# Optimization experiments

Measured on AMD Instinct MI355X. Metric: run time of the kernel, lower is better.

Reference implementation:

```python
import jax, jax.numpy as jnp
import numpy as np


def _gcn_smooth(X, src, dst, d_inv_sqrt, n):
    """Symmetric-normalized GCN smoothing: D^-1/2 (A + I) D^-1/2 X,
    with undirected edges given as (src, dst) pairs (applied both ways)."""
    norm = d_inv_sqrt[src] * d_inv_sqrt[dst]            # [E]
    out = jax.ops.segment_sum(X[src] * norm[:, None], dst, num_segments=n)
    out = out + jax.ops.segment_sum(X[dst] * norm[:, None], src, num_segments=n)
    out = out + X * (d_inv_sqrt * d_inv_sqrt)[:, None]  # self loops
    return out


def setup_inputs() -> dict:
    key = jax.random.key(0)
    k1, k2, k3, k4, k5 = jax.random.split(key, 5)
    N, E, C_in, C_hid, C_out = 50000, 800000, 128, 64, 40
    X = jax.random.normal(k1, (N, C_in), dtype=jnp.float32)
    edge_index = jax.random.randint(k2, (2, E), 0, N, dtype=jnp.int32)
    s1 = 1.0 / np.sqrt(C_in)
    s2 = 1.0 / np.sqrt(C_hid)
    W1 = jax.random.uniform(k3, (C_in, C_hid), jnp.float32, -s1, s1)
    b1 = jax.random.uniform(k4, (C_hid,), jnp.float32, -s1, s1)
    W2 = jax.random.uniform(k5, (C_hid, C_out), jnp.float32, -s2, s2)
    b2 = jax.random.uniform(jax.random.fold_in(key, 7), (C_out,), jnp.float32, -s2, s2)
    return {"X": X, "W1": W1, "b1": b1, "W2": W2, "b2": b2, "edge_index": edge_index}


def reference(X, W1, b1, W2, b2, edge_index):
    n = X.shape[0]
    src, dst = edge_index[0], edge_index[1]
    ones = jnp.ones(src.shape[0], dtype=X.dtype)
    deg = (1.0
           + jax.ops.segment_sum(ones, dst, num_segments=n)
           + jax.ops.segment_sum(ones, src, num_segments=n))  # deg of A + I
    d_inv_sqrt = jax.lax.rsqrt(deg)

    # Layer 1: theta -> smoothing -> relu (dropout is identity in eval)
    h = X @ W1 + b1
    h = _gcn_smooth(h, src, dst, d_inv_sqrt, n)
    out1 = jax.nn.relu(h)

    # Layer 2 (is_last): theta -> smoothing
    h2 = out1 @ W2 + b2
    out2 = _gcn_smooth(h2, src, dst, d_inv_sqrt, n)
    return (out1, out2)
```

## Files before the change

kernel.cpp:

```cpp
#include <hip/hip_runtime.h>


#define B1 256
#define BT 1024
#define GROWS 512
#define BUCK_SHIFT 6
#define CAP 4096
#define STAGE 8192
#define WK 136
#define WK2 72

typedef float f32x4 __attribute__((ext_vector_type(4)));
typedef short bf16x8 __attribute__((ext_vector_type(8)));

union Frag { unsigned int u[4]; bf16x8 v; };

__device__ __forceinline__ unsigned int cvt_pk_bf16(float a, float b) {
    unsigned int r;
    asm("v_cvt_pk_bf16_f32 %0, %1, %2" : "=v"(r) : "v"(a), "v"(b));
    return r;
}

__device__ __forceinline__ float bf_lo(unsigned int u) {
    return __uint_as_float(u << 16);
}
__device__ __forceinline__ float bf_hi(unsigned int u) {
    return __uint_as_float(u & 0xffff0000u);
}

__device__ __forceinline__ bf16x8 ld_frag(const unsigned short* p) {
    uint4 t = *reinterpret_cast<const uint4*>(p);
    Frag f; f.u[0] = t.x; f.u[1] = t.y; f.u[2] = t.z; f.u[3] = t.w;
    return f.v;
}

__device__ __forceinline__ void make_frags(const float4 a, const float4 b,
                                           bf16x8& hi8, bf16x8& lo8) {
    Frag hi, lo;
    hi.u[0] = cvt_pk_bf16(a.x, a.y);
    hi.u[1] = cvt_pk_bf16(a.z, a.w);
    hi.u[2] = cvt_pk_bf16(b.x, b.y);
    hi.u[3] = cvt_pk_bf16(b.z, b.w);
    lo.u[0] = cvt_pk_bf16(a.x - __uint_as_float(hi.u[0] << 16),
                          a.y - __uint_as_float(hi.u[0] & 0xffff0000u));
    lo.u[1] = cvt_pk_bf16(a.z - __uint_as_float(hi.u[1] << 16),
                          a.w - __uint_as_float(hi.u[1] & 0xffff0000u));
    lo.u[2] = cvt_pk_bf16(b.x - __uint_as_float(hi.u[2] << 16),
                          b.y - __uint_as_float(hi.u[2] & 0xffff0000u));
    lo.u[3] = cvt_pk_bf16(b.z - __uint_as_float(hi.u[3] << 16),
                          b.w - __uint_as_float(hi.u[3] & 0xffff0000u));
    hi8 = hi.v; lo8 = lo.v;
}

__global__ __launch_bounds__(BT) void k_build_gemm1(
        const int* __restrict__ src, const int* __restrict__ dst,
        int* __restrict__ cursors, unsigned int* __restrict__ binned,
        const float* __restrict__ X, const float* __restrict__ W1,
        const float* __restrict__ b1, unsigned short* __restrict__ hub,
        int E, int nbuck, int chunk, int N) {
    __shared__ __align__(16) char smem[49152];

    if (blockIdx.x < B1) {
        int* lh    = (int*)smem;
        int* lscan = lh + 1024;
        int* sbuf  = lscan + 1024;
        int* lbase = sbuf + 1024;
        unsigned int* stage = (unsigned int*)(lbase + 1024);

        const int t = threadIdx.x;
        lh[t] = 0;
        __syncthreads();

        int e0 = blockIdx.x * chunk;
        int e1 = min(e0 + chunk, E);
        int es[4], eds[4];
        #pragma unroll
        for (int i = 0; i < 4; ++i) {
            int e = e0 + t + i * BT;
            if (e < e1) {
                int s = src[e], d = dst[e];
                es[i] = s; eds[i] = d;
                atomicAdd(&lh[s >> BUCK_SHIFT], 1);
                atomicAdd(&lh[d >> BUCK_SHIFT], 1);
            }
        }
        __syncthreads();

        int cntv = lh[t];
        int* bufA = sbuf; int* bufB = lscan;
        bufA[t] = cntv;
        __syncthreads();
        #pragma unroll
        for (int w = 1; w < 1024; w <<= 1) {
            int x = bufA[t];
            if (t >= w) x += bufA[t - w];
            bufB[t] = x;
            __syncthreads();
            int* tmp = bufA; bufA = bufB; bufB = tmp;
        }
        int excl = bufA[t] - cntv;
        lscan[t] = excl;
        int rel = (t < nbuck && cntv > 0) ? atomicAdd(&cursors[t], cntv) : 0;
        lbase[t] = t * CAP + rel;
        lh[t] = excl;
        __syncthreads();

        #pragma unroll
        for (int i = 0; i < 4; ++i) {
            int e = e0 + t + i * BT;
            if (e < e1) {
                unsigned int s = (unsigned int)es[i];
                unsigned int d = (unsigned int)eds[i];
                int ps = atomicAdd(&lh[s >> BUCK_SHIFT], 1);
                stage[ps] = (s << 16) | d;
                int pd = atomicAdd(&lh[d >> BUCK_SHIFT], 1);
                stage[pd] = (d << 16) | s;
            }
        }
        __syncthreads();

        int total = 2 * (e1 - e0);
        for (int i = t; i < total; i += BT) {
            unsigned int v = stage[i];
            int b = (v >> 16) >> BUCK_SHIFT;
            int gpos = lbase[b] + (i - lscan[b]);
            if (gpos < ((b + 1) << 12)) binned[gpos] = v;
        }
        return;
    }

    unsigned short* sWhi = (unsigned short*)smem;
    unsigned short* sWlo = sWhi + 64 * WK;
    for (int i = threadIdx.x; i < 128 * 64; i += BT) {
        int c = i >> 7;
        int k = i & 127;
        float w = W1[(size_t)k * 64 + c];
        unsigned int hb = cvt_pk_bf16(w, 0.0f) & 0xffffu;
        float hf = __uint_as_float(hb << 16);
        unsigned int lb = cvt_pk_bf16(w - hf, 0.0f) & 0xffffu;
        sWhi[c * WK + k] = (unsigned short)hb;
        sWlo[c * WK + k] = (unsigned short)lb;
    }
    __syncthreads();

    const int lane = threadIdx.x & 63;
    const int wid  = threadIdx.x >> 6;
    const int ridx = lane & 15;
    const int kgrp = lane >> 4;
    const int r0 = (blockIdx.x - B1) * GROWS + wid * 32;

    f32x4 acc[2][4] = {};

    #pragma unroll
    for (int ks = 0; ks < 4; ++ks) {
        const int ka = ks * 32 + kgrp * 8;
        int ra0 = min(r0 + ridx, N - 1);
        int ra1 = min(r0 + 16 + ridx, N - 1);
        const float4* pa0 = (const float4*)(X + (size_t)ra0 * 128 + ka);
        const float4* pa1 = (const float4*)(X + (size_t)ra1 * 128 + ka);
        float4 a0a = pa0[0], a0b = pa0[1];
        float4 a1a = pa1[0], a1b = pa1[1];
        bf16x8 a0hi, a0lo, a1hi, a1lo;
        make_frags(a0a, a0b, a0hi, a0lo);
        make_frags(a1a, a1b, a1hi, a1lo);
        #pragma unroll
        for (int ct = 0; ct < 4; ++ct) {
            const int cbase = (ct * 16 + ridx) * WK + ka;
            bf16x8 bh = ld_frag(sWhi + cbase);
            bf16x8 bl = ld_frag(sWlo + cbase);
            acc[0][ct] = __builtin_amdgcn_mfma_f32_16x16x32_bf16(a0hi, bh, acc[0][ct], 0, 0, 0);
            acc[0][ct] = __builtin_amdgcn_mfma_f32_16x16x32_bf16(a0lo, bh, acc[0][ct], 0, 0, 0);
            acc[0][ct] = __builtin_amdgcn_mfma_f32_16x16x32_bf16(a0hi, bl, acc[0][ct], 0, 0, 0);
            acc[1][ct] = __builtin_amdgcn_mfma_f32_16x16x32_bf16(a1hi, bh, acc[1][ct], 0, 0, 0);
            acc[1][ct] = __builtin_amdgcn_mfma_f32_16x16x32_bf16(a1lo, bh, acc[1][ct], 0, 0, 0);
            acc[1][ct] = __builtin_amdgcn_mfma_f32_16x16x32_bf16(a1hi, bl, acc[1][ct], 0, 0, 0);
        }
    }

    float bias[4];
    #pragma unroll
    for (int ct = 0; ct < 4; ++ct) bias[ct] = b1[ct * 16 + ridx];

    #pragma unroll
    for (int rt = 0; rt < 2; ++rt) {
        int rb = r0 + rt * 16 + kgrp * 4;
        #pragma unroll
        for (int reg = 0; reg < 4; ++reg) {
            int r = rb + reg;
            if (r < N) {
                #pragma unroll
                for (int ct = 0; ct < 4; ++ct) {
                    float v = acc[rt][ct][reg] + bias[ct];
                    hub[(size_t)r * 64 + ct * 16 + ridx] =
                        (unsigned short)(cvt_pk_bf16(v, 0.0f) & 0xffffu);
                }
            }
        }
    }
}

__global__ __launch_bounds__(256) void k_reorder(const unsigned int* __restrict__ binned,
                                                 const int* __restrict__ cursors,
                                                 unsigned short* __restrict__ adj,
                                                 int* __restrict__ offs,
                                                 int* __restrict__ ends,
                                                 float* __restrict__ dis,
                                                 int N, int nbuck) {
    __shared__ int cnt[64];
    __shared__ int cur[64];
    __shared__ unsigned short stage[CAP];
    int b = blockIdx.x;
    int start = b * CAP;
    int fill = cursors[b]; if (fill > CAP) fill = CAP;
    int end = start + fill;
    if (threadIdx.x < 64) cnt[threadIdx.x] = 0;
    __syncthreads();
    unsigned int vv[16];
    #pragma unroll
    for (int i = 0; i < 16; ++i) {
        int idx = start + threadIdx.x + i * 256;
        if (idx < end) {
            unsigned int v = binned[idx];
            vv[i] = v;
            atomicAdd(&cnt[(v >> 16) & 63], 1);
        }
    }
    __syncthreads();
    if (threadIdx.x == 0) {
        int run = 0;
        for (int l = 0; l < 64; ++l) { cur[l] = run; run += cnt[l]; }
    }
    __syncthreads();
    if (threadIdx.x < 64) {
        int node = (b << BUCK_SHIFT) + threadIdx.x;
        if (node < N) {
            int o = start + cur[threadIdx.x];
            offs[node] = o;
            ends[node] = o + cnt[threadIdx.x];
            dis[node]  = rsqrtf(1.0f + (float)cnt[threadIdx.x]);
        }
    }
    __syncthreads();
    #pragma unroll
    for (int i = 0; i < 16; ++i) {
        int idx = start + threadIdx.x + i * 256;
        if (idx < end) {
            unsigned int v = vv[i];
            int nl = (v >> 16) & 63;
            int p = atomicAdd(&cur[nl], 1);
            stage[p] = (unsigned short)(v & 0xffffu);
        }
    }
    __syncthreads();
    for (int i = threadIdx.x; i < fill; i += 256)
        adj[start + i] = stage[i];
}

__global__ __launch_bounds__(256) void k_gather64(const unsigned int* __restrict__ hsu,
                                                  const unsigned short* __restrict__ adj,
                                                  const int* __restrict__ offs,
                                                  const int* __restrict__ ends,
                                                  const float* __restrict__ dis,
                                                  float* __restrict__ out1, int N) {
    int node = (blockIdx.x * 256 + threadIdx.x) >> 6;
    if (node >= N) return;
    int lane = threadIdx.x & 63;
    int half = lane >> 5;
    int c2 = lane & 31;
    int k   = offs[node];
    int end = ends[node];
    float acc0 = 0.f, acc1 = 0.f;
    for (; k + 16 <= end; k += 16) {
        int j0 = adj[k +  0 + half], j1 = adj[k +  2 + half];
        int j2 = adj[k +  4 + half], j3 = adj[k +  6 + half];
        int j4 = adj[k +  8 + half], j5 = adj[k + 10 + half];
        int j6 = adj[k + 12 + half], j7 = adj[k + 14 + half];
        float d0 = dis[j0], d1 = dis[j1], d2 = dis[j2], d3 = dis[j3];
        float d4 = dis[j4], d5 = dis[j5], d6 = dis[j6], d7 = dis[j7];
        unsigned int u0 = hsu[(size_t)j0 * 32 + c2];
        unsigned int u1 = hsu[(size_t)j1 * 32 + c2];
        unsigned int u2 = hsu[(size_t)j2 * 32 + c2];
        unsigned int u3 = hsu[(size_t)j3 * 32 + c2];
        unsigned int u4 = hsu[(size_t)j4 * 32 + c2];
        unsigned int u5 = hsu[(size_t)j5 * 32 + c2];
        unsigned int u6 = hsu[(size_t)j6 * 32 + c2];
        unsigned int u7 = hsu[(size_t)j7 * 32 + c2];
        acc0 = fmaf(d0, bf_lo(u0), acc0); acc1 = fmaf(d0, bf_hi(u0), acc1);
        acc0 = fmaf(d1, bf_lo(u1), acc0); acc1 = fmaf(d1, bf_hi(u1), acc1);
        acc0 = fmaf(d2, bf_lo(u2), acc0); acc1 = fmaf(d2, bf_hi(u2), acc1);
        acc0 = fmaf(d3, bf_lo(u3), acc0); acc1 = fmaf(d3, bf_hi(u3), acc1);
        acc0 = fmaf(d4, bf_lo(u4), acc0); acc1 = fmaf(d4, bf_hi(u4), acc1);
        acc0 = fmaf(d5, bf_lo(u5), acc0); acc1 = fmaf(d5, bf_hi(u5), acc1);
        acc0 = fmaf(d6, bf_lo(u6), acc0); acc1 = fmaf(d6, bf_hi(u6), acc1);
        acc0 = fmaf(d7, bf_lo(u7), acc0); acc1 = fmaf(d7, bf_hi(u7), acc1);
    }
    for (; k + 8 <= end; k += 8) {
        int j0 = adj[k + 0 + half], j1 = adj[k + 2 + half];
        int j2 = adj[k + 4 + half], j3 = adj[k + 6 + half];
        float d0 = dis[j0], d1 = dis[j1], d2 = dis[j2], d3 = dis[j3];
        unsigned int u0 = hsu[(size_t)j0 * 32 + c2];
        unsigned int u1 = hsu[(size_t)j1 * 32 + c2];
        unsigned int u2 = hsu[(size_t)j2 * 32 + c2];
        unsigned int u3 = hsu[(size_t)j3 * 32 + c2];
        acc0 = fmaf(d0, bf_lo(u0), acc0); acc1 = fmaf(d0, bf_hi(u0), acc1);
        acc0 = fmaf(d1, bf_lo(u1), acc0); acc1 = fmaf(d1, bf_hi(u1), acc1);
        acc0 = fmaf(d2, bf_lo(u2), acc0); acc1 = fmaf(d2, bf_hi(u2), acc1);
        acc0 = fmaf(d3, bf_lo(u3), acc0); acc1 = fmaf(d3, bf_hi(u3), acc1);
    }
    for (; k + 2 <= end; k += 2) {
        int j = adj[k + half];
        float d = dis[j];
        unsigned int u = hsu[(size_t)j * 32 + c2];
        acc0 = fmaf(d, bf_lo(u), acc0);
        acc1 = fmaf(d, bf_hi(u), acc1);
    }
    if (k < end && half == 0) {
        int j = adj[k];
        float d = dis[j];
        unsigned int u = hsu[(size_t)j * 32 + c2];
        acc0 = fmaf(d, bf_lo(u), acc0);
        acc1 = fmaf(d, bf_hi(u), acc1);
    }
    acc0 += __shfl_xor(acc0, 32);
    acc1 += __shfl_xor(acc1, 32);
    float d = dis[node];
    unsigned int us = hsu[(size_t)node * 32 + c2];
    acc0 = fmaf(d, bf_lo(us), acc0);
    acc1 = fmaf(d, bf_hi(us), acc1);
    if (half == 0) {
        float2 r;
        r.x = fmaxf(d * acc0, 0.0f);
        r.y = fmaxf(d * acc1, 0.0f);
        *reinterpret_cast<float2*>(out1 + (size_t)node * 64 + 2 * c2) = r;
    }
}

__global__ __launch_bounds__(256) void k_gemm2_mfma(const float* __restrict__ A,
                                                    const float* __restrict__ W2,
                                                    const float* __restrict__ b2,
                                                    const float* __restrict__ dis,
                                                    unsigned short* __restrict__ h2sb,
                                                    int N) {
    __shared__ unsigned short sWhi[48 * WK2];
    __shared__ unsigned short sWlo[48 * WK2];
    for (int i = threadIdx.x; i < 48 * 64; i += 256) {
        int c = i >> 6;
        int k = i & 63;
        float w = (c < 40) ? W2[(size_t)k * 40 + c] : 0.0f;
        unsigned int hb = cvt_pk_bf16(w, 0.0f) & 0xffffu;
        float hf = __uint_as_float(hb << 16);
        unsigned int lb = cvt_pk_bf16(w - hf, 0.0f) & 0xffffu;
        sWhi[c * WK2 + k] = (unsigned short)hb;
        sWlo[c * WK2 + k] = (unsigned short)lb;
    }
    __syncthreads();

    const int lane = threadIdx.x & 63;
    const int wid  = threadIdx.x >> 6;
    const int ridx = lane & 15;
    const int kgrp = lane >> 4;
    const int r0 = blockIdx.x * 128 + wid * 32;
    if (r0 >= N) return;

    f32x4 acc[2][3] = {};

    #pragma unroll
    for (int ks = 0; ks < 2; ++ks) {
        const int ka = ks * 32 + kgrp * 8;
        int ra0 = min(r0 + ridx, N - 1);
        int ra1 = min(r0 + 16 + ridx, N - 1);
        const float4* pa0 = (const float4*)(A + (size_t)ra0 * 64 + ka);
        const float4* pa1 = (const float4*)(A + (size_t)ra1 * 64 + ka);
        float4 a0a = pa0[0], a0b = pa0[1];
        float4 a1a = pa1[0], a1b = pa1[1];
        bf16x8 a0hi, a0lo, a1hi, a1lo;
        make_frags(a0a, a0b, a0hi, a0lo);
        make_frags(a1a, a1b, a1hi, a1lo);
        #pragma unroll
        for (int ct = 0; ct < 3; ++ct) {
            const int cbase = (ct * 16 + ridx) * WK2 + ka;
            bf16x8 bh = ld_frag(sWhi + cbase);
            bf16x8 bl = ld_frag(sWlo + cbase);
            acc[0][ct] = __builtin_amdgcn_mfma_f32_16x16x32_bf16(a0hi, bh, acc[0][ct], 0, 0, 0);
            acc[0][ct] = __builtin_amdgcn_mfma_f32_16x16x32_bf16(a0lo, bh, acc[0][ct], 0, 0, 0);
            acc[0][ct] = __builtin_amdgcn_mfma_f32_16x16x32_bf16(a0hi, bl, acc[0][ct], 0, 0, 0);
            acc[1][ct] = __builtin_amdgcn_mfma_f32_16x16x32_bf16(a1hi, bh, acc[1][ct], 0, 0, 0);
            acc[1][ct] = __builtin_amdgcn_mfma_f32_16x16x32_bf16(a1lo, bh, acc[1][ct], 0, 0, 0);
            acc[1][ct] = __builtin_amdgcn_mfma_f32_16x16x32_bf16(a1hi, bl, acc[1][ct], 0, 0, 0);
        }
    }

    float bias[3];
    #pragma unroll
    for (int ct = 0; ct < 3; ++ct) {
        int c = ct * 16 + ridx;
        bias[ct] = (c < 40) ? b2[c] : 0.0f;
    }

    #pragma unroll
    for (int rt = 0; rt < 2; ++rt) {
        int rb = r0 + rt * 16 + kgrp * 4;
        #pragma unroll
        for (int reg = 0; reg < 4; ++reg) {
            int r = rb + reg;
            if (r < N) {
                float dv = dis[r];
                #pragma unroll
                for (int ct = 0; ct < 3; ++ct) {
                    int c = ct * 16 + ridx;
                    if (c < 40) {
                        float v = (acc[rt][ct][reg] + bias[ct]) * dv;
                        h2sb[(size_t)r * 40 + c] =
                            (unsigned short)(cvt_pk_bf16(v, 0.0f) & 0xffffu);
                    }
                }
            }
        }
    }
}

__global__ __launch_bounds__(256) void k_gather40(const unsigned int* __restrict__ h2u,
                                                  const unsigned short* __restrict__ adj,
                                                  const int* __restrict__ offs,
                                                  const int* __restrict__ ends,
                                                  const float* __restrict__ dis,
                                                  float* __restrict__ out, int N) {
    int node = (blockIdx.x * 256 + threadIdx.x) >> 6;
    if (node >= N) return;
    int lane = threadIdx.x & 63;
    int g = lane / 20;
    int c = lane - g * 20;
    bool act = g < 3;
    int k   = offs[node];
    int end = ends[node];
    float acc0 = 0.f, acc1 = 0.f;
    for (; k + 6 <= end; k += 6) {
        if (act) {
            int ja = adj[k + g];
            int jb = adj[k + 3 + g];
            unsigned int ua = h2u[(size_t)ja * 20 + c];
            unsigned int ub = h2u[(size_t)jb * 20 + c];
            acc0 += bf_lo(ua) + bf_lo(ub);
            acc1 += bf_hi(ua) + bf_hi(ub);
        }
    }
    for (; k + 3 <= end; k += 3) {
        if (act) {
            int j = adj[k + g];
            unsigned int u = h2u[(size_t)j * 20 + c];
            acc0 += bf_lo(u);
            acc1 += bf_hi(u);
        }
    }
    int rem = end - k;
    if (act && g < rem) {
        int j = adj[k + g];
        unsigned int u = h2u[(size_t)j * 20 + c];
        acc0 += bf_lo(u);
        acc1 += bf_hi(u);
    }
    acc0 += __shfl(acc0, lane + 20) + __shfl(acc0, lane + 40);
    acc1 += __shfl(acc1, lane + 20) + __shfl(acc1, lane + 40);
    if (lane < 20) {
        unsigned int us = h2u[(size_t)node * 20 + c];
        float d = dis[node];
        float2 r;
        r.x = d * (acc0 + bf_lo(us));
        r.y = d * (acc1 + bf_hi(us));
        *reinterpret_cast<float2*>(out + (size_t)node * 40 + 2 * c) = r;
    }
}

extern "C" void kernel_launch(void* const* d_in, const int* in_sizes, int n_in,
                              void* d_out, int out_size, void* d_ws, size_t ws_size,
                              hipStream_t stream) {
    const float* X  = (const float*)d_in[0];
    const float* W1 = (const float*)d_in[1];
    const float* b1 = (const float*)d_in[2];
    const float* W2 = (const float*)d_in[3];
    const float* b2 = (const float*)d_in[4];
    const int*   ei = (const int*)d_in[5];

    const int Chid = in_sizes[2];
    const int Cin  = in_sizes[1] / Chid;
    const int N    = in_sizes[0] / Cin;
    const int E    = in_sizes[5] / 2;

    const int* src = ei;
    const int* dst = ei + E;

    const int nbuck = (N + 63) >> BUCK_SHIFT;
    const int chunk = (E + B1 - 1) / B1;
    const size_t slots = (size_t)nbuck * CAP;

    auto align256 = [](size_t x) { return (x + 255) & ~(size_t)255; };
    char* p = (char*)d_ws;
    int*   cursors = (int*)p; p += align256((size_t)nbuck * 4);
    float* dis     = (float*)p; p += align256((size_t)N * 4);
    int*   offs    = (int*)p; p += align256((size_t)N * 4);
    int*   ends    = (int*)p; p += align256((size_t)N * 4);
    unsigned short* adj = (unsigned short*)p; p += align256(slots * 2);
    unsigned int* binned = (unsigned int*)p; p += align256(slots * 4);
    unsigned int* h2u    = binned;
    unsigned short* hub  = (unsigned short*)p;

    float* out1 = (float*)d_out;
    float* out2 = out1 + (size_t)N * 64;

    hipMemsetAsync(cursors, 0, (size_t)nbuck * 4, stream);

    const int gemmBlocks = (N + GROWS - 1) / GROWS;
    k_build_gemm1<<<B1 + gemmBlocks, BT, 0, stream>>>(src, dst, cursors, binned,
                                                      X, W1, b1, hub,
                                                      E, nbuck, chunk, N);
    k_reorder<<<nbuck, 256, 0, stream>>>(binned, cursors, adj, offs, ends, dis,
                                         N, nbuck);
    k_gather64<<<(N + 3) / 4, 256, 0, stream>>>((const unsigned int*)hub, adj,
                                                offs, ends, dis, out1, N);
    k_gemm2_mfma<<<(N + 127) / 128, 256, 0, stream>>>(out1, W2, b2, dis,
                                                      (unsigned short*)h2u, N);
    k_gather40<<<(N + 3) / 4, 256, 0, stream>>>(h2u, adj, offs, ends, dis, out2, N);
}
```

Before: 121.1 us.

## Fuse layer-1 gather with layer-2 GEMM through shared-memory row tile

Merges the layer-1 neighbor gather (with ReLU) and the second linear layer into one kernel. Each 1024-thread block gathers 64 nodes, stages the activated rows and their degree scale in LDS, then computes the 64x40 projection with scalar FP32 FMAs against W2 held in LDS. This removes one kernel launch and the re-read of out1 from global memory. In exchange it drops the MFMA path for GEMM2 and adds a block barrier that couples the 16 waves, so load imbalance across nodes with different degrees can leave waves idle.

```diff
diff --git a/kernel.cpp b/kernel.cpp
--- a/kernel.cpp
+++ b/kernel.cpp
@@ -8,7 +8,6 @@
 #define CAP 4096
 #define STAGE 8192
 #define WK 136
-#define WK2 72
 
 typedef float f32x4 __attribute__((ext_vector_type(4)));
 typedef short bf16x8 __attribute__((ext_vector_type(8)));
@@ -256,164 +255,119 @@
         adj[start + i] = stage[i];
 }
 
-__global__ __launch_bounds__(256) void k_gather64(const unsigned int* __restrict__ hsu,
-                                                  const unsigned short* __restrict__ adj,
-                                                  const int* __restrict__ offs,
-                                                  const int* __restrict__ ends,
-                                                  const float* __restrict__ dis,
-                                                  float* __restrict__ out1, int N) {
-    int node = (blockIdx.x * 256 + threadIdx.x) >> 6;
-    if (node >= N) return;
-    int lane = threadIdx.x & 63;
-    int half = lane >> 5;
-    int c2 = lane & 31;
-    int k   = offs[node];
-    int end = ends[node];
-    float acc0 = 0.f, acc1 = 0.f;
-    for (; k + 16 <= end; k += 16) {
-        int j0 = adj[k +  0 + half], j1 = adj[k +  2 + half];
-        int j2 = adj[k +  4 + half], j3 = adj[k +  6 + half];
-        int j4 = adj[k +  8 + half], j5 = adj[k + 10 + half];
-        int j6 = adj[k + 12 + half], j7 = adj[k + 14 + half];
-        float d0 = dis[j0], d1 = dis[j1], d2 = dis[j2], d3 = dis[j3];
-        float d4 = dis[j4], d5 = dis[j5], d6 = dis[j6], d7 = dis[j7];
-        unsigned int u0 = hsu[(size_t)j0 * 32 + c2];
-        unsigned int u1 = hsu[(size_t)j1 * 32 + c2];
-        unsigned int u2 = hsu[(size_t)j2 * 32 + c2];
-        unsigned int u3 = hsu[(size_t)j3 * 32 + c2];
-        unsigned int u4 = hsu[(size_t)j4 * 32 + c2];
-        unsigned int u5 = hsu[(size_t)j5 * 32 + c2];
-        unsigned int u6 = hsu[(size_t)j6 * 32 + c2];
-        unsigned int u7 = hsu[(size_t)j7 * 32 + c2];
-        acc0 = fmaf(d0, bf_lo(u0), acc0); acc1 = fmaf(d0, bf_hi(u0), acc1);
-        acc0 = fmaf(d1, bf_lo(u1), acc0); acc1 = fmaf(d1, bf_hi(u1), acc1);
-        acc0 = fmaf(d2, bf_lo(u2), acc0); acc1 = fmaf(d2, bf_hi(u2), acc1);
-        acc0 = fmaf(d3, bf_lo(u3), acc0); acc1 = fmaf(d3, bf_hi(u3), acc1);
-        acc0 = fmaf(d4, bf_lo(u4), acc0); acc1 = fmaf(d4, bf_hi(u4), acc1);
-        acc0 = fmaf(d5, bf_lo(u5), acc0); acc1 = fmaf(d5, bf_hi(u5), acc1);
-        acc0 = fmaf(d6, bf_lo(u6), acc0); acc1 = fmaf(d6, bf_hi(u6), acc1);
-        acc0 = fmaf(d7, bf_lo(u7), acc0); acc1 = fmaf(d7, bf_hi(u7), acc1);
-    }
-    for (; k + 8 <= end; k += 8) {
-        int j0 = adj[k + 0 + half], j1 = adj[k + 2 + half];
-        int j2 = adj[k + 4 + half], j3 = adj[k + 6 + half];
-        float d0 = dis[j0], d1 = dis[j1], d2 = dis[j2], d3 = dis[j3];
-        unsigned int u0 = hsu[(size_t)j0 * 32 + c2];
-        unsigned int u1 = hsu[(size_t)j1 * 32 + c2];
-        unsigned int u2 = hsu[(size_t)j2 * 32 + c2];
-        unsigned int u3 = hsu[(size_t)j3 * 32 + c2];
-        acc0 = fmaf(d0, bf_lo(u0), acc0); acc1 = fmaf(d0, bf_hi(u0), acc1);
-        acc0 = fmaf(d1, bf_lo(u1), acc0); acc1 = fmaf(d1, bf_hi(u1), acc1);
-        acc0 = fmaf(d2, bf_lo(u2), acc0); acc1 = fmaf(d2, bf_hi(u2), acc1);
-        acc0 = fmaf(d3, bf_lo(u3), acc0); acc1 = fmaf(d3, bf_hi(u3), acc1);
-    }
-    for (; k + 2 <= end; k += 2) {
-        int j = adj[k + half];
-        float d = dis[j];
-        unsigned int u = hsu[(size_t)j * 32 + c2];
-        acc0 = fmaf(d, bf_lo(u), acc0);
-        acc1 = fmaf(d, bf_hi(u), acc1);
-    }
-    if (k < end && half == 0) {
-        int j = adj[k];
-        float d = dis[j];
-        unsigned int u = hsu[(size_t)j * 32 + c2];
-        acc0 = fmaf(d, bf_lo(u), acc0);
-        acc1 = fmaf(d, bf_hi(u), acc1);
-    }
-    acc0 += __shfl_xor(acc0, 32);
-    acc1 += __shfl_xor(acc1, 32);
-    float d = dis[node];
-    unsigned int us = hsu[(size_t)node * 32 + c2];
-    acc0 = fmaf(d, bf_lo(us), acc0);
-    acc1 = fmaf(d, bf_hi(us), acc1);
-    if (half == 0) {
-        float2 r;
-        r.x = fmaxf(d * acc0, 0.0f);
-        r.y = fmaxf(d * acc1, 0.0f);
-        *reinterpret_cast<float2*>(out1 + (size_t)node * 64 + 2 * c2) = r;
-    }
-}
-
-__global__ __launch_bounds__(256) void k_gemm2_mfma(const float* __restrict__ A,
-                                                    const float* __restrict__ W2,
-                                                    const float* __restrict__ b2,
-                                                    const float* __restrict__ dis,
-                                                    unsigned short* __restrict__ h2sb,
-                                                    int N) {
-    __shared__ unsigned short sWhi[48 * WK2];
-    __shared__ unsigned short sWlo[48 * WK2];
-    for (int i = threadIdx.x; i < 48 * 64; i += 256) {
-        int c = i >> 6;
-        int k = i & 63;
-        float w = (c < 40) ? W2[(size_t)k * 40 + c] : 0.0f;
-        unsigned int hb = cvt_pk_bf16(w, 0.0f) & 0xffffu;
-        float hf = __uint_as_float(hb << 16);
-        unsigned int lb = cvt_pk_bf16(w - hf, 0.0f) & 0xffffu;
-        sWhi[c * WK2 + k] = (unsigned short)hb;
-        sWlo[c * WK2 + k] = (unsigned short)lb;
-    }
-    __syncthreads();
-
+__global__ __launch_bounds__(BT) void k_gather64_g2(
+        const unsigned int* __restrict__ hsu,
+        const unsigned short* __restrict__ adj,
+        const int* __restrict__ offs, const int* __restrict__ ends,
+        const float* __restrict__ dis,
+        const float* __restrict__ W2, const float* __restrict__ b2,
+        float* __restrict__ out1, unsigned short* __restrict__ h2sb, int N) {
+    __shared__ float sW[64 * 40];
+    __shared__ float sb[40];
+    __shared__ float srow[64][66];
+
+    for (int i = threadIdx.x; i < 64 * 40; i += BT) sW[i] = W2[i];
+    if (threadIdx.x < 40) sb[threadIdx.x] = b2[threadIdx.x];
+
+    const int wave = threadIdx.x >> 6;
     const int lane = threadIdx.x & 63;
-    const int wid  = threadIdx.x >> 6;
-    const int ridx = lane & 15;
-    const int kgrp = lane >> 4;
-    const int r0 = blockIdx.x * 128 + wid * 32;
-    if (r0 >= N) return;
-
-    f32x4 acc[2][3] = {};
-
-    #pragma unroll
-    for (int ks = 0; ks < 2; ++ks) {
-        const int ka = ks * 32 + kgrp * 8;
-        int ra0 = min(r0 + ridx, N - 1);
-        int ra1 = min(r0 + 16 + ridx, N - 1);
-        const float4* pa0 = (const float4*)(A + (size_t)ra0 * 64 + ka);
-        const float4* pa1 = (const float4*)(A + (size_t)ra1 * 64 + ka);
-        float4 a0a = pa0[0], a0b = pa0[1];
-        float4 a1a = pa1[0], a1b = pa1[1];
-        bf16x8 a0hi, a0lo, a1hi, a1lo;
-        make_frags(a0a, a0b, a0hi, a0lo);
-        make_frags(a1a, a1b, a1hi, a1lo);
-        #pragma unroll
-        for (int ct = 0; ct < 3; ++ct) {
-            const int cbase = (ct * 16 + ridx) * WK2 + ka;
-            bf16x8 bh = ld_frag(sWhi + cbase);
-            bf16x8 bl = ld_frag(sWlo + cbase);
-            acc[0][ct] = __builtin_amdgcn_mfma_f32_16x16x32_bf16(a0hi, bh, acc[0][ct], 0, 0, 0);
-            acc[0][ct] = __builtin_amdgcn_mfma_f32_16x16x32_bf16(a0lo, bh, acc[0][ct], 0, 0, 0);
-            acc[0][ct] = __builtin_amdgcn_mfma_f32_16x16x32_bf16(a0hi, bl, acc[0][ct], 0, 0, 0);
-            acc[1][ct] = __builtin_amdgcn_mfma_f32_16x16x32_bf16(a1hi, bh, acc[1][ct], 0, 0, 0);
-            acc[1][ct] = __builtin_amdgcn_mfma_f32_16x16x32_bf16(a1lo, bh, acc[1][ct], 0, 0, 0);
-            acc[1][ct] = __builtin_amdgcn_mfma_f32_16x16x32_bf16(a1hi, bl, acc[1][ct], 0, 0, 0);
-        }
-    }
-
-    float bias[3];
-    #pragma unroll
-    for (int ct = 0; ct < 3; ++ct) {
-        int c = ct * 16 + ridx;
-        bias[ct] = (c < 40) ? b2[c] : 0.0f;
-    }
-
-    #pragma unroll
-    for (int rt = 0; rt < 2; ++rt) {
-        int rb = r0 + rt * 16 + kgrp * 4;
-        #pragma unroll
-        for (int reg = 0; reg < 4; ++reg) {
-            int r = rb + reg;
-            if (r < N) {
-                float dv = dis[r];
+    const int half = lane >> 5;
+    const int c2 = lane & 31;
+    const int base = blockIdx.x * 64;
+
+    #pragma unroll
+    for (int q = 0; q < 4; ++q) {
+        int row = wave * 4 + q;
+        int node = base + row;
+        if (node < N) {
+            int k   = offs[node];
+            int end = ends[node];
+            float acc0 = 0.f, acc1 = 0.f;
+            for (; k + 16 <= end; k += 16) {
+                int j0 = adj[k +  0 + half], j1 = adj[k +  2 + half];
+                int j2 = adj[k +  4 + half], j3 = adj[k +  6 + half];
+                int j4 = adj[k +  8 + half], j5 = adj[k + 10 + half];
+                int j6 = adj[k + 12 + half], j7 = adj[k + 14 + half];
+                float d0 = dis[j0], d1 = dis[j1], d2 = dis[j2], d3 = dis[j3];
+                float d4 = dis[j4], d5 = dis[j5], d6 = dis[j6], d7 = dis[j7];
+                unsigned int u0 = hsu[(size_t)j0 * 32 + c2];
+                unsigned int u1 = hsu[(size_t)j1 * 32 + c2];
+                unsigned int u2 = hsu[(size_t)j2 * 32 + c2];
+                unsigned int u3 = hsu[(size_t)j3 * 32 + c2];
+                unsigned int u4 = hsu[(size_t)j4 * 32 + c2];
+                unsigned int u5 = hsu[(size_t)j5 * 32 + c2];
+                unsigned int u6 = hsu[(size_t)j6 * 32 + c2];
+                unsigned int u7 = hsu[(size_t)j7 * 32 + c2];
+                acc0 = fmaf(d0, bf_lo(u0), acc0); acc1 = fmaf(d0, bf_hi(u0), acc1);
+                acc0 = fmaf(d1, bf_lo(u1), acc0); acc1 = fmaf(d1, bf_hi(u1), acc1);
+                acc0 = fmaf(d2, bf_lo(u2), acc0); acc1 = fmaf(d2, bf_hi(u2), acc1);
+                acc0 = fmaf(d3, bf_lo(u3), acc0); acc1 = fmaf(d3, bf_hi(u3), acc1);
+                acc0 = fmaf(d4, bf_lo(u4), acc0); acc1 = fmaf(d4, bf_hi(u4), acc1);
+                acc0 = fmaf(d5, bf_lo(u5), acc0); acc1 = fmaf(d5, bf_hi(u5), acc1);
+                acc0 = fmaf(d6, bf_lo(u6), acc0); acc1 = fmaf(d6, bf_hi(u6), acc1);
+                acc0 = fmaf(d7, bf_lo(u7), acc0); acc1 = fmaf(d7, bf_hi(u7), acc1);
+            }
+            for (; k + 8 <= end; k += 8) {
+                int j0 = adj[k + 0 + half], j1 = adj[k + 2 + half];
+                int j2 = adj[k + 4 + half], j3 = adj[k + 6 + half];
+                float d0 = dis[j0], d1 = dis[j1], d2 = dis[j2], d3 = dis[j3];
+                unsigned int u0 = hsu[(size_t)j0 * 32 + c2];
+                unsigned int u1 = hsu[(size_t)j1 * 32 + c2];
+                unsigned int u2 = hsu[(size_t)j2 * 32 + c2];
+                unsigned int u3 = hsu[(size_t)j3 * 32 + c2];
+                acc0 = fmaf(d0, bf_lo(u0), acc0); acc1 = fmaf(d0, bf_hi(u0), acc1);
+                acc0 = fmaf(d1, bf_lo(u1), acc0); acc1 = fmaf(d1, bf_hi(u1), acc1);
+                acc0 = fmaf(d2, bf_lo(u2), acc0); acc1 = fmaf(d2, bf_hi(u2), acc1);
+                acc0 = fmaf(d3, bf_lo(u3), acc0); acc1 = fmaf(d3, bf_hi(u3), acc1);
+            }
+            for (; k + 2 <= end; k += 2) {
+                int j = adj[k + half];
+                float d = dis[j];
+                unsigned int u = hsu[(size_t)j * 32 + c2];
+                acc0 = fmaf(d, bf_lo(u), acc0);
+                acc1 = fmaf(d, bf_hi(u), acc1);
+            }
+            if (k < end && half == 0) {
+                int j = adj[k];
+                float d = dis[j];
+                unsigned int u = hsu[(size_t)j * 32 + c2];
+                acc0 = fmaf(d, bf_lo(u), acc0);
+                acc1 = fmaf(d, bf_hi(u), acc1);
+            }
+            acc0 += __shfl_xor(acc0, 32);
+            acc1 += __shfl_xor(acc1, 32);
+            float d = dis[node];
+            unsigned int us = hsu[(size_t)node * 32 + c2];
+            acc0 = fmaf(d, bf_lo(us), acc0);
+            acc1 = fmaf(d, bf_hi(us), acc1);
+            if (half == 0) {
+                float v0 = fmaxf(d * acc0, 0.0f);
+                float v1 = fmaxf(d * acc1, 0.0f);
+                float2 r; r.x = v0; r.y = v1;
+                *reinterpret_cast<float2*>(out1 + (size_t)node * 64 + 2 * c2) = r;
+                *reinterpret_cast<float2*>(&srow[row][2 * c2]) = r;
+                if (c2 == 0) srow[row][64] = d;
+            }
+        }
+    }
+    __syncthreads();
+
+    const int col = threadIdx.x & 63;
+    const int rr  = threadIdx.x >> 6;
+    if (col < 40) {
+        #pragma unroll
+        for (int pass = 0; pass < 4; ++pass) {
+            int row = pass * 16 + rr;
+            int node = base + row;
+            if (node < N) {
+                float acc = sb[col];
+                const float* rp = srow[row];
                 #pragma unroll
-                for (int ct = 0; ct < 3; ++ct) {
-                    int c = ct * 16 + ridx;
-                    if (c < 40) {
-                        float v = (acc[rt][ct][reg] + bias[ct]) * dv;
-                        h2sb[(size_t)r * 40 + c] =
-                            (unsigned short)(cvt_pk_bf16(v, 0.0f) & 0xffffu);
-                    }
-                }
+                for (int k = 0; k < 64; ++k)
+                    acc = fmaf(rp[k], sW[k * 40 + col], acc);
+                float v = acc * rp[64];
+                h2sb[(size_t)node * 40 + col] =
+                    (unsigned short)(cvt_pk_bf16(v, 0.0f) & 0xffffu);
             }
         }
     }
@@ -515,9 +469,8 @@
                                                       E, nbuck, chunk, N);
     k_reorder<<<nbuck, 256, 0, stream>>>(binned, cursors, adj, offs, ends, dis,
                                          N, nbuck);
-    k_gather64<<<(N + 3) / 4, 256, 0, stream>>>((const unsigned int*)hub, adj,
-                                                offs, ends, dis, out1, N);
-    k_gemm2_mfma<<<(N + 127) / 128, 256, 0, stream>>>(out1, W2, b2, dis,
-                                                      (unsigned short*)h2u, N);
+    k_gather64_g2<<<nbuck, BT, 0, stream>>>((const unsigned int*)hub, adj,
+                                            offs, ends, dis, W2, b2,
+                                            out1, (unsigned short*)h2u, N);
     k_gather40<<<(N + 3) / 4, 256, 0, stream>>>(h2u, adj, offs, ends, dis, out2, N);
 }
```

New measurement: 143.9 us. +18.9%, slower.
